# Kernel optimization log

Hardware: AMD Instinct MI355X
Metric: run time of the kernel (lower is better)

## Reference

```python
import jax, jax.numpy as jnp
import numpy as np

EPS = 1e-7
MAX_TANH = 15.0
C = 1.0  # curvature of every PoincareBall manifold in the stack

def _norm(x):
    return jnp.clip(jnp.linalg.norm(x, axis=-1, keepdims=True), EPS, None)

def _artanh(x):
    return jnp.arctanh(jnp.clip(x, -1.0 + 1e-5, 1.0 - 1e-5))

def proj(x, c=C):
    # clip points back inside the Poincare ball
    maxnorm = (1.0 - 1e-5) / jnp.sqrt(c)
    n = _norm(x)
    return jnp.where(n > maxnorm, x / n * maxnorm, x)

def expmap0(u, c=C):
    sc = jnp.sqrt(c)
    n = _norm(u)
    return jnp.tanh(jnp.clip(sc * n, -MAX_TANH, MAX_TANH)) * u / (sc * n)

def logmap0(x, c=C):
    sc = jnp.sqrt(c)
    n = _norm(x)
    return _artanh(sc * n) * x / (sc * n)

def mobius_add(x, y, c=C):
    x2 = jnp.sum(x * x, -1, keepdims=True)
    y2 = jnp.sum(y * y, -1, keepdims=True)
    xy = jnp.sum(x * y, -1, keepdims=True)
    num = (1 + 2 * c * xy + c * y2) * x + (1 - c * x2) * y
    den = 1 + 2 * c * xy + c * c * x2 * y2
    return num / jnp.clip(den, EPS, None)

def mobius_matvec(W, x, c=C):
    sc = jnp.sqrt(c)
    xn = _norm(x)
    mx = x @ W.T
    mxn = _norm(mx)
    return jnp.tanh(jnp.clip(mxn / xn * _artanh(sc * xn), -MAX_TANH, MAX_TANH)) * mx / (mxn * sc)

def hgc_layer(x, edges, node_mask, edge_mask, W, b, c_in=C, c_out=C):
    n_nodes = x.shape[0]
    # HypLinear: mobius matvec + hyperbolic bias add
    h = proj(mobius_matvec(W, x, c_in), c_in)
    hyp_bias = proj(expmap0(b[None, :], c_in), c_in)
    h = proj(mobius_add(h, hyp_bias, c_in), c_in)
    # HypAgg: masked tangent-space mean over incoming edges (gather -> segment_sum)
    row, col = edges[0], edges[1]
    ht = logmap0(h, c_in)                 # [N, d] tangent features
    msgs = ht[col] * edge_mask            # [E, d]
    agg = jax.ops.segment_sum(msgs, row, num_segments=n_nodes)
    deg = jax.ops.segment_sum(edge_mask, row, num_segments=n_nodes)
    agg = agg / jnp.clip(deg, 1.0, None)
    h = proj(expmap0(agg, c_in), c_in)
    # HypAct: nonlinearity in tangent space, re-map to output manifold
    xt = jax.nn.relu(logmap0(h, c_in))
    h = proj(expmap0(xt, c_out), c_out)
    return h * node_mask

N_NODES = 50000
N_EDGES = 1200000
DIM = 64
NUM_LAYERS = 2

def setup_inputs() -> dict:
    key = jax.random.key(0)
    ks = jax.random.split(key, 8)
    h_tan = 0.1 * jax.random.normal(ks[0], (N_NODES, DIM), dtype=jnp.float32)
    h = proj(expmap0(h_tan))  # valid Poincare-ball points
    distances = jax.random.uniform(ks[1], (N_EDGES, 1), dtype=jnp.float32)
    edges = jax.random.randint(ks[2], (2, N_EDGES), 0, N_NODES, dtype=jnp.int64)
    node_mask = jnp.ones((N_NODES, 1), dtype=jnp.float32)
    edge_mask = jnp.ones((N_EDGES, 1), dtype=jnp.float32)
    W0 = 0.1 * jax.random.normal(ks[3], (DIM, DIM), dtype=jnp.float32)
    b0 = 0.01 * jax.random.normal(ks[4], (DIM,), dtype=jnp.float32)
    W1 = 0.1 * jax.random.normal(ks[5], (DIM, DIM), dtype=jnp.float32)
    b1 = 0.01 * jax.random.normal(ks[6], (DIM,), dtype=jnp.float32)
    return {"h": h, "distances": distances, "edges": edges,
            "node_mask": node_mask, "edge_mask": edge_mask,
            "W0": W0, "b0": b0, "W1": W1, "b1": b1}

def reference(h, distances, edges, node_mask, edge_mask, W0, b0, W1, b1):
    # nn.Sequential of HyperbolicGraphConvolution layers; distances/edges/masks pass through
    out = hgc_layer(h, edges, node_mask, edge_mask, W0, b0)
    out = hgc_layer(out, edges, node_mask, edge_mask, W1, b1)
    return out
```

## Files before the change

kernel.cpp:

```cpp
#include <hip/hip_runtime.h>
#include <hip/hip_fp16.h>

#define EPS      1e-7f
#define MAX_TANH 15.0f
#define MAXNORM  0.99999f
#define ART_CLIP 0.99999f
#define HGRID    512
#define RPB      64
#define RPB_SHIFT 6
#define CAPF     2048
#define NBMAX    1024

__device__ __forceinline__ float frcp(float x) {
    return __builtin_amdgcn_rcpf(x);
}

__device__ __forceinline__ float fast_tanh_pos(float x) {
    float e = __expf(-2.0f * x);
    return (1.0f - e) * frcp(1.0f + e);
}

__device__ __forceinline__ float clamp_tanh_arg(float x) {
    return fminf(fmaxf(x, -MAX_TANH), MAX_TANH);
}

__device__ __forceinline__ float artanh_clip(float x) {
    x = fminf(fmaxf(x, -ART_CLIP), ART_CLIP);
    return 0.5f * __logf((1.0f + x) * frcp(1.0f - x));
}

__device__ __forceinline__ float gsum16(float v) {
    v += __shfl_xor(v, 1, 64);
    v += __shfl_xor(v, 2, 64);
    v += __shfl_xor(v, 4, 64);
    v += __shfl_xor(v, 8, 64);
    return v;
}

__device__ __forceinline__ void fma_h4(float4& acc, uint2 u, float m) {
    float2 f01 = __half22float2(*reinterpret_cast<__half2*>(&u.x));
    float2 f23 = __half22float2(*reinterpret_cast<__half2*>(&u.y));
    acc.x = fmaf(f01.x, m, acc.x); acc.y = fmaf(f01.y, m, acc.y);
    acc.z = fmaf(f23.x, m, acc.z); acc.w = fmaf(f23.y, m, acc.w);
}

__device__ __forceinline__ float rec_mask(unsigned v) {
    unsigned short hb = (unsigned short)(v >> 16);
    return __half2float(*reinterpret_cast<__half*>(&hb));
}

__global__ __launch_bounds__(256) void hist_kernel(
    const int* __restrict__ rows, unsigned short* __restrict__ histB,
    int n_edges, int epb, int nb)
{
    __shared__ int hh[NBMAX];
    const int b0 = blockIdx.x * epb;
    const int b1 = min(b0 + epb, n_edges);
    for (int j = threadIdx.x; j < nb; j += 256) hh[j] = 0;
    __syncthreads();
    for (int i = b0 + threadIdx.x; i < b1; i += 256)
        atomicAdd(&hh[rows[i] >> RPB_SHIFT], 1);
    __syncthreads();
    for (int j = threadIdx.x; j < nb; j += 256)
        histB[blockIdx.x * nb + j] = (unsigned short)hh[j];
}

__global__ __launch_bounds__(256, 4) void transform_kernel(
    const float* __restrict__ x, const float* __restrict__ W,
    const float* __restrict__ b, __half* __restrict__ ht, int n_nodes)
{
    __shared__ float WT[4096];
    __shared__ float xs[16 * 68];

    const int t = threadIdx.x;
    const int q = t & 15;
    const int g = t >> 4;

#pragma unroll
    for (int r = 0; r < 16; ++r) {
        int idx = r * 256 + t;
        int j = idx >> 6, k = idx & 63;
        WT[(k << 6) | (j ^ ((k & 15) << 2))] = W[idx];
    }

    float4 b4 = ((const float4*)b)[q];
    float ssb = b4.x*b4.x + b4.y*b4.y + b4.z*b4.z + b4.w*b4.w;
    float bn = fmaxf(sqrtf(gsum16(ssb)), EPS);
    float tb = fast_tanh_pos(clamp_tanh_arg(bn));
    float sb = tb * frcp(bn);
    float4 hb4 = make_float4(b4.x * sb, b4.y * sb, b4.z * sb, b4.w * sb);
    if (tb > MAXNORM) {
        float sc = MAXNORM * frcp(tb);
        hb4.x *= sc; hb4.y *= sc; hb4.z *= sc; hb4.w *= sc;
        tb = MAXNORM;
    }
    const float y2 = tb * tb;
    __syncthreads();

    const int node = blockIdx.x * 16 + g;
    const bool valid = node < n_nodes;
    const int nd = valid ? node : 0;

    float* xrow = &xs[g * 68];

    float4 x4 = ((const float4*)(x + (long long)nd * 64))[q];
    *(float4*)(xrow + (q << 2)) = x4;

    float ssx = x4.x*x4.x + x4.y*x4.y + x4.z*x4.z + x4.w*x4.w;
    float xn = fmaxf(sqrtf(gsum16(ssx)), EPS);

    float4 mxa = make_float4(0.f, 0.f, 0.f, 0.f);
    float4 mxb = make_float4(0.f, 0.f, 0.f, 0.f);
#pragma unroll
    for (int k = 0; k < 64; k += 2) {
        float xk0 = xrow[k], xk1 = xrow[k + 1];
        const float4 w0 = *(const float4*)&WT[((k    ) << 6) | ((q << 2) ^ (((k    ) & 15) << 2))];
        const float4 w1 = *(const float4*)&WT[((k + 1) << 6) | ((q << 2) ^ (((k + 1) & 15) << 2))];
        mxa.x = fmaf(w0.x, xk0, mxa.x); mxa.y = fmaf(w0.y, xk0, mxa.y);
        mxa.z = fmaf(w0.z, xk0, mxa.z); mxa.w = fmaf(w0.w, xk0, mxa.w);
        mxb.x = fmaf(w1.x, xk1, mxb.x); mxb.y = fmaf(w1.y, xk1, mxb.y);
        mxb.z = fmaf(w1.z, xk1, mxb.z); mxb.w = fmaf(w1.w, xk1, mxb.w);
    }
    float4 mx = make_float4(mxa.x + mxb.x, mxa.y + mxb.y,
                            mxa.z + mxb.z, mxa.w + mxb.w);

    float ssm = mx.x*mx.x + mx.y*mx.y + mx.z*mx.z + mx.w*mx.w;
    float mxn = fmaxf(sqrtf(gsum16(ssm)), EPS);
    float r = fast_tanh_pos(clamp_tanh_arg(mxn * frcp(xn) * artanh_clip(xn)));
    float rs = r * frcp(mxn);
    float4 hj = make_float4(mx.x * rs, mx.y * rs, mx.z * rs, mx.w * rs);
    float hn = fmaxf(r, EPS);
    if (hn > MAXNORM) {
        float sc = MAXNORM * frcp(hn);
        hj.x *= sc; hj.y *= sc; hj.z *= sc; hj.w *= sc;
        hn = MAXNORM;
    }

    float x2 = hn * hn;
    float xy = gsum16(hj.x*hb4.x + hj.y*hb4.y + hj.z*hb4.z + hj.w*hb4.w);
    float ca = 1.0f + 2.0f * xy + y2;
    float cb = 1.0f - x2;
    float iden = frcp(fmaxf(1.0f + 2.0f * xy + x2 * y2, EPS));
    hj.x = (ca * hj.x + cb * hb4.x) * iden;
    hj.y = (ca * hj.y + cb * hb4.y) * iden;
    hj.z = (ca * hj.z + cb * hb4.z) * iden;
    hj.w = (ca * hj.w + cb * hb4.w) * iden;

    float ssh = hj.x*hj.x + hj.y*hj.y + hj.z*hj.z + hj.w*hj.w;
    float hn2 = fmaxf(sqrtf(gsum16(ssh)), EPS);
    float sc2 = (hn2 > MAXNORM) ? (MAXNORM * frcp(hn2)) : 1.0f;
    float hnc = fminf(hn2, MAXNORM);
    float lr = artanh_clip(hnc) * frcp(hnc) * sc2;
    hj.x *= lr; hj.y *= lr; hj.z *= lr; hj.w *= lr;

    if (valid) {
        __half2 p01 = __float22half2_rn(make_float2(hj.x, hj.y));
        __half2 p23 = __float22half2_rn(make_float2(hj.z, hj.w));
        uint2 o;
        o.x = *reinterpret_cast<unsigned*>(&p01);
        o.y = *reinterpret_cast<unsigned*>(&p23);
        *((uint2*)(ht + (long long)node * 64) + q) = o;
    }
}

__global__ __launch_bounds__(HGRID) void scan_bucket_kernel(
    unsigned short* __restrict__ histB, int* __restrict__ tot, int nb)
{
    __shared__ int wsum[8];
    const int b = blockIdx.x;
    const int t = threadIdx.x;
    const int lane = t & 63, wid = t >> 6;
    int v = histB[t * nb + b];
    int incl = v;
#pragma unroll
    for (int o = 1; o < 64; o <<= 1) {
        int tt = __shfl_up(incl, o, 64);
        if (lane >= o) incl += tt;
    }
    if (lane == 63) wsum[wid] = incl;
    __syncthreads();
    if (wid == 0 && lane < 8) {
        int ws = wsum[lane];
#pragma unroll
        for (int o = 1; o < 8; o <<= 1) {
            int tt = __shfl_up(ws, o, 64);
            if (lane >= o) ws += tt;
        }
        wsum[lane] = ws;
    }
    __syncthreads();
    int base = (wid > 0) ? wsum[wid - 1] : 0;
    histB[t * nb + b] = (unsigned short)(base + incl - v);
    if (t == HGRID - 1) tot[b] = base + incl;
}

__global__ __launch_bounds__(NBMAX) void scan_base_kernel(
    const int* __restrict__ tot, int* __restrict__ bucket_base, int nb)
{
    __shared__ int s[NBMAX];
    const int t = threadIdx.x;
    int v = (t < nb) ? tot[t] : 0;
    s[t] = v;
    __syncthreads();
    for (int off = 1; off < NBMAX; off <<= 1) {
        int u = (t >= off) ? s[t - off] : 0;
        __syncthreads();
        s[t] += u;
        __syncthreads();
    }
    if (t < nb) bucket_base[t] = s[t] - v;
    if (t == nb - 1) bucket_base[nb] = s[t];
}

__global__ __launch_bounds__(256) void coarse_scatter_kernel(
    const int* __restrict__ rows, const int* __restrict__ cols,
    const float* __restrict__ edge_mask, const unsigned short* __restrict__ off,
    const int* __restrict__ bucket_base,
    int2* __restrict__ coarse, int n_edges, int epb, int nb)
{
    __shared__ int cur[NBMAX];
    const int b0 = blockIdx.x * epb;
    const int b1 = min(b0 + epb, n_edges);
    for (int j = threadIdx.x; j < nb; j += 256)
        cur[j] = bucket_base[j] + (int)off[blockIdx.x * nb + j];
    __syncthreads();
    for (int i = b0 + threadIdx.x; i < b1; i += 256) {
        int r = rows[i], c = cols[i];
        float m = edge_mask[i];
        int pos = atomicAdd(&cur[r >> RPB_SHIFT], 1);
        coarse[pos] = make_int2((r << 16) | c, __float_as_int(m));
    }
}

__global__ __launch_bounds__(512) void fine_gather_kernel(
    const int2* __restrict__ coarse, const int* __restrict__ bucket_base,
    const __half* __restrict__ ht1, const float* __restrict__ node_mask,
    const float* __restrict__ W, const float* __restrict__ bvec,
    unsigned* __restrict__ csr4, int* __restrict__ row_start,
    __half* __restrict__ ht2, int n_nodes, int n_edges)
{
    __shared__ int hh[RPB], incl[RPB], curs[RPB];
    __shared__ unsigned outE[CAPF];
    __shared__ float WT[4096];
    __shared__ float xs[32 * 68];

    const int t = threadIdx.x;
    const int b = blockIdx.x;
    const int q = t & 15;
    const int g = t >> 4;
    const int bbase = bucket_base[b];
    const int n_e = bucket_base[b + 1] - bbase;

#pragma unroll
    for (int r = 0; r < 8; ++r) {
        int idx = r * 512 + t;
        int j = idx >> 6, k = idx & 63;
        WT[(k << 6) | (j ^ ((k & 15) << 2))] = W[idx];
    }
    float4 b4 = ((const float4*)bvec)[q];
    float ssb = b4.x*b4.x + b4.y*b4.y + b4.z*b4.z + b4.w*b4.w;
    float bn = fmaxf(sqrtf(gsum16(ssb)), EPS);
    float tb = fast_tanh_pos(clamp_tanh_arg(bn));
    float sb = tb * frcp(bn);
    float4 hb4 = make_float4(b4.x * sb, b4.y * sb, b4.z * sb, b4.w * sb);
    if (tb > MAXNORM) {
        float sc = MAXNORM * frcp(tb);
        hb4.x *= sc; hb4.y *= sc; hb4.z *= sc; hb4.w *= sc;
        tb = MAXNORM;
    }
    const float y2 = tb * tb;

    if (t < RPB) hh[t] = 0;
    __syncthreads();
    int2 regs[4];
#pragma unroll
    for (int k = 0; k < 4; ++k) {
        int i = t + k * 512;
        if (i < n_e) {
            regs[k] = coarse[bbase + i];
            atomicAdd(&hh[(regs[k].x >> 16) & (RPB - 1)], 1);
        }
    }
    __syncthreads();
    if (t < 64) {
        int v = hh[t];
        int inc = v;
#pragma unroll
        for (int o = 1; o < 64; o <<= 1) {
            int tt = __shfl_up(inc, o, 64);
            if (t >= o) inc += tt;
        }
        incl[t] = inc;
        curs[t] = inc - v;
        int grow = (b << RPB_SHIFT) + t;
        if (grow < n_nodes) row_start[grow] = bbase + inc - v;
    }
    if (b == gridDim.x - 1 && t == 0) row_start[n_nodes] = n_edges;
    __syncthreads();
#pragma unroll
    for (int k = 0; k < 4; ++k) {
        int i = t + k * 512;
        if (i < n_e) {
            int slot = atomicAdd(&curs[(regs[k].x >> 16) & (RPB - 1)], 1);
            if (slot < CAPF) {
                __half hm = __float2half(__int_as_float(regs[k].y));
                outE[slot] = (unsigned)(regs[k].x & 0xffff) |
                             ((unsigned)*reinterpret_cast<unsigned short*>(&hm) << 16);
            }
        }
    }
    __syncthreads();

    const int lim = min(n_e, CAPF);
    for (int i = t; i < lim; i += 512)
        csr4[bbase + i] = outE[i];

    const uint2* __restrict__ htq = (const uint2*)ht1 + q;

#pragma unroll
    for (int batch = 0; batch < 2; ++batch) {
        const int ln = batch * 32 + g;
        const int node = (b << RPB_SHIFT) + ln;
        const bool valid = node < n_nodes;
        const int nd = valid ? node : (n_nodes - 1);
        const int s0 = incl[ln] - hh[ln];
        const int e0 = incl[ln];

        float4 acc = make_float4(0.f, 0.f, 0.f, 0.f);
        float msum = 0.f;
        int j = s0;
        for (; j + 8 <= e0; j += 8) {
            unsigned v0 = outE[j    ], v1 = outE[j + 1], v2 = outE[j + 2], v3 = outE[j + 3];
            unsigned v4 = outE[j + 4], v5 = outE[j + 5], v6 = outE[j + 6], v7 = outE[j + 7];
            uint2 u0 = htq[(v0 & 0xffffu) * 16u];
            uint2 u1 = htq[(v1 & 0xffffu) * 16u];
            uint2 u2 = htq[(v2 & 0xffffu) * 16u];
            uint2 u3 = htq[(v3 & 0xffffu) * 16u];
            uint2 u4 = htq[(v4 & 0xffffu) * 16u];
            uint2 u5 = htq[(v5 & 0xffffu) * 16u];
            uint2 u6 = htq[(v6 & 0xffffu) * 16u];
            uint2 u7 = htq[(v7 & 0xffffu) * 16u];
            float m0 = rec_mask(v0), m1 = rec_mask(v1);
            float m2 = rec_mask(v2), m3 = rec_mask(v3);
            float m4 = rec_mask(v4), m5 = rec_mask(v5);
            float m6 = rec_mask(v6), m7 = rec_mask(v7);
            fma_h4(acc, u0, m0); fma_h4(acc, u1, m1);
            fma_h4(acc, u2, m2); fma_h4(acc, u3, m3);
            fma_h4(acc, u4, m4); fma_h4(acc, u5, m5);
            fma_h4(acc, u6, m6); fma_h4(acc, u7, m7);
            msum += (m0 + m1 + m2 + m3) + (m4 + m5 + m6 + m7);
        }
        for (; j + 4 <= e0; j += 4) {
            unsigned v0 = outE[j], v1 = outE[j + 1], v2 = outE[j + 2], v3 = outE[j + 3];
            uint2 u0 = htq[(v0 & 0xffffu) * 16u];
            uint2 u1 = htq[(v1 & 0xffffu) * 16u];
            uint2 u2 = htq[(v2 & 0xffffu) * 16u];
            uint2 u3 = htq[(v3 & 0xffffu) * 16u];
            float m0 = rec_mask(v0), m1 = rec_mask(v1);
            float m2 = rec_mask(v2), m3 = rec_mask(v3);
            fma_h4(acc, u0, m0); fma_h4(acc, u1, m1);
            fma_h4(acc, u2, m2); fma_h4(acc, u3, m3);
            msum += m0 + m1 + m2 + m3;
        }
        for (; j < e0; ++j) {
            unsigned v = outE[j];
            uint2 u = htq[(v & 0xffffu) * 16u];
            float m = rec_mask(v);
            fma_h4(acc, u, m);
            msum += m;
        }

        const float inv = frcp(fmaxf(msum, 1.0f));
        acc.x *= inv; acc.y *= inv; acc.z *= inv; acc.w *= inv;

        float ss = acc.x*acc.x + acc.y*acc.y + acc.z*acc.z + acc.w*acc.w;
        float n1 = fmaxf(sqrtf(gsum16(ss)), EPS);
        float t1 = fast_tanh_pos(clamp_tanh_arg(n1));
        float r1 = t1 * frcp(n1);
        acc.x *= r1; acc.y *= r1; acc.z *= r1; acc.w *= r1;
        if (t1 > MAXNORM) {
            float sc = MAXNORM * frcp(t1);
            acc.x *= sc; acc.y *= sc; acc.z *= sc; acc.w *= sc;
            t1 = MAXNORM;
        }
        float n2 = fmaxf(t1, EPS);
        float r2s = artanh_clip(n2) * frcp(n2);
        acc.x = fmaxf(acc.x * r2s, 0.f); acc.y = fmaxf(acc.y * r2s, 0.f);
        acc.z = fmaxf(acc.z * r2s, 0.f); acc.w = fmaxf(acc.w * r2s, 0.f);

        ss = acc.x*acc.x + acc.y*acc.y + acc.z*acc.z + acc.w*acc.w;
        float n3 = fmaxf(sqrtf(gsum16(ss)), EPS);
        float t3 = fast_tanh_pos(clamp_tanh_arg(n3));
        float r3 = t3 * frcp(n3);
        acc.x *= r3; acc.y *= r3; acc.z *= r3; acc.w *= r3;
        if (t3 > MAXNORM) {
            float sc = MAXNORM * frcp(t3);
            acc.x *= sc; acc.y *= sc; acc.z *= sc; acc.w *= sc;
            t3 = MAXNORM;
        }

        const float nm = node_mask[nd];
        acc.x *= nm; acc.y *= nm; acc.z *= nm; acc.w *= nm;

        float* xrow = &xs[g * 68];
        *(float4*)(xrow + (q << 2)) = acc;

        float4 mxa = make_float4(0.f, 0.f, 0.f, 0.f);
        float4 mxb = make_float4(0.f, 0.f, 0.f, 0.f);
#pragma unroll
        for (int k = 0; k < 64; k += 2) {
            float xk0 = xrow[k], xk1 = xrow[k + 1];
            const float4 w0 = *(const float4*)&WT[((k    ) << 6) | ((q << 2) ^ (((k    ) & 15) << 2))];
            const float4 w1 = *(const float4*)&WT[((k + 1) << 6) | ((q << 2) ^ (((k + 1) & 15) << 2))];
            mxa.x = fmaf(w0.x, xk0, mxa.x); mxa.y = fmaf(w0.y, xk0, mxa.y);
            mxa.z = fmaf(w0.z, xk0, mxa.z); mxa.w = fmaf(w0.w, xk0, mxa.w);
            mxb.x = fmaf(w1.x, xk1, mxb.x); mxb.y = fmaf(w1.y, xk1, mxb.y);
            mxb.z = fmaf(w1.z, xk1, mxb.z); mxb.w = fmaf(w1.w, xk1, mxb.w);
        }
        float4 mx = make_float4(mxa.x + mxb.x, mxa.y + mxb.y,
                                mxa.z + mxb.z, mxa.w + mxb.w);

        float xn  = fmaxf(t3 * fabsf(nm), EPS);
        float ssm = mx.x*mx.x + mx.y*mx.y + mx.z*mx.z + mx.w*mx.w;
        float mxn = fmaxf(sqrtf(gsum16(ssm)), EPS);
        float r = fast_tanh_pos(clamp_tanh_arg(mxn * frcp(xn) * artanh_clip(xn)));
        float rs = r * frcp(mxn);
        float4 hj = make_float4(mx.x * rs, mx.y * rs, mx.z * rs, mx.w * rs);
        float hn = fmaxf(r, EPS);
        if (hn > MAXNORM) {
            float sc = MAXNORM * frcp(hn);
            hj.x *= sc; hj.y *= sc; hj.z *= sc; hj.w *= sc;
            hn = MAXNORM;
        }

        float x2 = hn * hn;
        float xy = gsum16(hj.x*hb4.x + hj.y*hb4.y + hj.z*hb4.z + hj.w*hb4.w);
        float ca = 1.0f + 2.0f * xy + y2;
        float cb = 1.0f - x2;
        float iden = frcp(fmaxf(1.0f + 2.0f * xy + x2 * y2, EPS));
        hj.x = (ca * hj.x + cb * hb4.x) * iden;
        hj.y = (ca * hj.y + cb * hb4.y) * iden;
        hj.z = (ca * hj.z + cb * hb4.z) * iden;
        hj.w = (ca * hj.w + cb * hb4.w) * iden;

        float ssh = hj.x*hj.x + hj.y*hj.y + hj.z*hj.z + hj.w*hj.w;
        float hn2 = fmaxf(sqrtf(gsum16(ssh)), EPS);
        float sc2 = (hn2 > MAXNORM) ? (MAXNORM * frcp(hn2)) : 1.0f;
        float hnc = fminf(hn2, MAXNORM);
        float lr = artanh_clip(hnc) * frcp(hnc) * sc2;
        hj.x *= lr; hj.y *= lr; hj.z *= lr; hj.w *= lr;

        if (valid) {
            __half2 p01 = __float22half2_rn(make_float2(hj.x, hj.y));
            __half2 p23 = __float22half2_rn(make_float2(hj.z, hj.w));
            uint2 o;
            o.x = *reinterpret_cast<unsigned*>(&p01);
            o.y = *reinterpret_cast<unsigned*>(&p23);
            *((uint2*)(ht2 + (long long)node * 64) + q) = o;
        }
    }
}

__global__ __launch_bounds__(256) void gather2_kernel(
    const __half* __restrict__ ht, const unsigned* __restrict__ csr4,
    const int* __restrict__ row_start, const float* __restrict__ node_mask,
    float* __restrict__ outp, int n_nodes)
{
    const int t = threadIdx.x;
    const int lane = t & 63;
    const int wv = t >> 6;
    const int ns = lane >> 4;
    const int q  = lane & 15;

    const int node = blockIdx.x * 16 + (wv << 2) + ns;
    const bool valid = node < n_nodes;
    const int nd = valid ? node : (n_nodes - 1);
    const int s = row_start[nd];
    const int e = row_start[nd + 1];

    const uint2* __restrict__ htq = (const uint2*)ht + q;

    float4 acc = make_float4(0.f, 0.f, 0.f, 0.f);
    float msum = 0.f;
    int j = s;
    for (; j + 8 <= e; j += 8) {
        unsigned v0 = csr4[j    ], v1 = csr4[j + 1], v2 = csr4[j + 2], v3 = csr4[j + 3];
        unsigned v4 = csr4[j + 4], v5 = csr4[j + 5], v6 = csr4[j + 6], v7 = csr4[j + 7];
        uint2 u0 = htq[(v0 & 0xffffu) * 16u];
        uint2 u1 = htq[(v1 & 0xffffu) * 16u];
        uint2 u2 = htq[(v2 & 0xffffu) * 16u];
        uint2 u3 = htq[(v3 & 0xffffu) * 16u];
        uint2 u4 = htq[(v4 & 0xffffu) * 16u];
        uint2 u5 = htq[(v5 & 0xffffu) * 16u];
        uint2 u6 = htq[(v6 & 0xffffu) * 16u];
        uint2 u7 = htq[(v7 & 0xffffu) * 16u];
        float m0 = rec_mask(v0), m1 = rec_mask(v1);
        float m2 = rec_mask(v2), m3 = rec_mask(v3);
        float m4 = rec_mask(v4), m5 = rec_mask(v5);
        float m6 = rec_mask(v6), m7 = rec_mask(v7);
        fma_h4(acc, u0, m0); fma_h4(acc, u1, m1);
        fma_h4(acc, u2, m2); fma_h4(acc, u3, m3);
        fma_h4(acc, u4, m4); fma_h4(acc, u5, m5);
        fma_h4(acc, u6, m6); fma_h4(acc, u7, m7);
        msum += (m0 + m1 + m2 + m3) + (m4 + m5 + m6 + m7);
    }
    for (; j + 4 <= e; j += 4) {
        unsigned v0 = csr4[j], v1 = csr4[j + 1], v2 = csr4[j + 2], v3 = csr4[j + 3];
        uint2 u0 = htq[(v0 & 0xffffu) * 16u];
        uint2 u1 = htq[(v1 & 0xffffu) * 16u];
        uint2 u2 = htq[(v2 & 0xffffu) * 16u];
        uint2 u3 = htq[(v3 & 0xffffu) * 16u];
        float m0 = rec_mask(v0), m1 = rec_mask(v1);
        float m2 = rec_mask(v2), m3 = rec_mask(v3);
        fma_h4(acc, u0, m0); fma_h4(acc, u1, m1);
        fma_h4(acc, u2, m2); fma_h4(acc, u3, m3);
        msum += m0 + m1 + m2 + m3;
    }
    for (; j < e; ++j) {
        unsigned v = csr4[j];
        uint2 u = htq[(v & 0xffffu) * 16u];
        float m = rec_mask(v);
        fma_h4(acc, u, m);
        msum += m;
    }

    const float inv = frcp(fmaxf(msum, 1.0f));
    acc.x *= inv; acc.y *= inv; acc.z *= inv; acc.w *= inv;

    float ss = acc.x*acc.x + acc.y*acc.y + acc.z*acc.z + acc.w*acc.w;
    float n1 = fmaxf(sqrtf(gsum16(ss)), EPS);
    float t1 = fast_tanh_pos(clamp_tanh_arg(n1));
    float r1 = t1 * frcp(n1);
    acc.x *= r1; acc.y *= r1; acc.z *= r1; acc.w *= r1;
    if (t1 > MAXNORM) {
        float sc = MAXNORM * frcp(t1);
        acc.x *= sc; acc.y *= sc; acc.z *= sc; acc.w *= sc;
        t1 = MAXNORM;
    }
    float n2 = fmaxf(t1, EPS);
    float r2 = artanh_clip(n2) * frcp(n2);
    acc.x = fmaxf(acc.x * r2, 0.f); acc.y = fmaxf(acc.y * r2, 0.f);
    acc.z = fmaxf(acc.z * r2, 0.f); acc.w = fmaxf(acc.w * r2, 0.f);

    ss = acc.x*acc.x + acc.y*acc.y + acc.z*acc.z + acc.w*acc.w;
    float n3 = fmaxf(sqrtf(gsum16(ss)), EPS);
    float t3 = fast_tanh_pos(clamp_tanh_arg(n3));
    float r3 = t3 * frcp(n3);
    acc.x *= r3; acc.y *= r3; acc.z *= r3; acc.w *= r3;
    if (t3 > MAXNORM) {
        float sc = MAXNORM * frcp(t3);
        acc.x *= sc; acc.y *= sc; acc.z *= sc; acc.w *= sc;
        t3 = MAXNORM;
    }

    const float nm = node_mask[nd];
    acc.x *= nm; acc.y *= nm; acc.z *= nm; acc.w *= nm;

    if (valid) ((float4*)(outp + (long long)node * 64))[q] = acc;
}

extern "C" void kernel_launch(void* const* d_in, const int* in_sizes, int n_in,
                              void* d_out, int out_size, void* d_ws, size_t ws_size,
                              hipStream_t stream) {
    const float* h         = (const float*)d_in[0];
    const int*   edges     = (const int*)d_in[2];
    const float* node_mask = (const float*)d_in[3];
    const float* edge_mask = (const float*)d_in[4];
    const float* W0        = (const float*)d_in[5];
    const float* b0        = (const float*)d_in[6];
    const float* W1        = (const float*)d_in[7];
    const float* b1        = (const float*)d_in[8];
    float* out = (float*)d_out;

    const int N = in_sizes[0] / 64;
    const int E = in_sizes[4];
    const int* rows = edges;
    const int* cols = edges + E;

    const int NB  = (N + RPB - 1) / RPB;
    const int EPB = (E + HGRID - 1) / HGRID;

    size_t nd = (size_t)N * 64;
    char* ws = (char*)d_ws;
    __half*   B1          = (__half*)ws;   ws += nd * sizeof(__half);
    __half*   B2          = (__half*)ws;   ws += nd * sizeof(__half);
    int2*     coarse      = (int2*)ws;     ws += (size_t)E * sizeof(int2);
    unsigned* csr4        = (unsigned*)ws; ws += (size_t)E * sizeof(unsigned);
    unsigned short* histB = (unsigned short*)ws;
    ws += (size_t)HGRID * NB * sizeof(unsigned short);
    int*      tot         = (int*)ws;      ws += (size_t)NB * sizeof(int);
    int*      bucket_base = (int*)ws;      ws += (size_t)(NB + 1) * sizeof(int);
    int*      row_start   = (int*)ws;      ws += (size_t)(N + 1) * sizeof(int);

    const int TB = (N + 15) / 16;
    const int NGRID = (N + 15) / 16;

    hist_kernel<<<HGRID, 256, 0, stream>>>(rows, histB, E, EPB, NB);

    transform_kernel<<<TB, 256, 0, stream>>>(h, W0, b0, B1, N);

    scan_bucket_kernel<<<NB, HGRID, 0, stream>>>(histB, tot, NB);
    scan_base_kernel<<<1, NBMAX, 0, stream>>>(tot, bucket_base, NB);

    coarse_scatter_kernel<<<HGRID, 256, 0, stream>>>(
        rows, cols, edge_mask, histB, bucket_base, coarse, E, EPB, NB);

    fine_gather_kernel<<<NB, 512, 0, stream>>>(
        coarse, bucket_base, B1, node_mask, W1, b1, csr4, row_start, B2, N, E);

    gather2_kernel<<<NGRID, 256, 0, stream>>>(
        B2, csr4, row_start, node_mask, out, N);
}
```

Measured before the change: 195.9 us.

## Replace bucketed two-pass CSR build with global atomic count/scan/scatter

Replaces the hierarchical bucket histogram plus coarse scatter plus in-LDS fine sort with a direct per-node count using global atomics, a three-kernel prefix scan, and a global-atomic scatter into CSR. The first-layer gather, previously fused with the fine sort, becomes a standalone gather1 kernel that reads the CSR, mirroring gather2. This removes the intermediate coarse buffer and shared-memory bucketing. In exchange it adds heavy global atomic contention on per-node counters and cursors, scatters edges in nondeterministic order, and adds more kernel launches.

```diff
diff --git a/kernel.cpp b/kernel.cpp
--- a/kernel.cpp
+++ b/kernel.cpp
@@ -5,11 +5,6 @@
 #define MAX_TANH 15.0f
 #define MAXNORM  0.99999f
 #define ART_CLIP 0.99999f
-#define HGRID    512
-#define RPB      64
-#define RPB_SHIFT 6
-#define CAPF     2048
-#define NBMAX    1024
 
 __device__ __forceinline__ float frcp(float x) {
     return __builtin_amdgcn_rcpf(x);
@@ -49,20 +44,80 @@
     return __half2float(*reinterpret_cast<__half*>(&hb));
 }
 
-__global__ __launch_bounds__(256) void hist_kernel(
-    const int* __restrict__ rows, unsigned short* __restrict__ histB,
-    int n_edges, int epb, int nb)
-{
-    __shared__ int hh[NBMAX];
-    const int b0 = blockIdx.x * epb;
-    const int b1 = min(b0 + epb, n_edges);
-    for (int j = threadIdx.x; j < nb; j += 256) hh[j] = 0;
+__global__ __launch_bounds__(256) void zero_kernel(int* __restrict__ p, int n)
+{
+    int i = blockIdx.x * 256 + threadIdx.x;
+    if (i < n) p[i] = 0;
+}
+
+__global__ __launch_bounds__(256) void count_kernel(
+    const int* __restrict__ rows, int* __restrict__ cnt, int n_edges)
+{
+    const int stride = gridDim.x * 256;
+    for (int i = blockIdx.x * 256 + threadIdx.x; i < n_edges; i += stride)
+        atomicAdd(&cnt[rows[i]], 1);
+}
+
+__global__ __launch_bounds__(1024) void scanA_kernel(
+    const int* __restrict__ cnt, int* __restrict__ rs,
+    int* __restrict__ partial, int n)
+{
+    __shared__ int s[1024];
+    const int t = threadIdx.x;
+    const int i = blockIdx.x * 1024 + t;
+    int v = (i < n) ? cnt[i] : 0;
+    s[t] = v;
     __syncthreads();
-    for (int i = b0 + threadIdx.x; i < b1; i += 256)
-        atomicAdd(&hh[rows[i] >> RPB_SHIFT], 1);
-    __syncthreads();
-    for (int j = threadIdx.x; j < nb; j += 256)
-        histB[blockIdx.x * nb + j] = (unsigned short)hh[j];
+    for (int off = 1; off < 1024; off <<= 1) {
+        int u = (t >= off) ? s[t - off] : 0;
+        __syncthreads();
+        s[t] += u;
+        __syncthreads();
+    }
+    if (i < n) rs[i] = s[t] - v;
+    if (t == 1023) partial[blockIdx.x] = s[1023];
+}
+
+__global__ __launch_bounds__(64) void scanB_kernel(
+    int* __restrict__ partial, int nch)
+{
+    const int t = threadIdx.x;
+    int v = (t < nch) ? partial[t] : 0;
+    int inc = v;
+#pragma unroll
+    for (int o = 1; o < 64; o <<= 1) {
+        int u = __shfl_up(inc, o, 64);
+        if (t >= o) inc += u;
+    }
+    if (t < nch) partial[t] = inc - v;
+}
+
+__global__ __launch_bounds__(256) void scanC_kernel(
+    int* __restrict__ rs, int* __restrict__ cursor,
+    const int* __restrict__ partial, int n, int e)
+{
+    int i = blockIdx.x * 256 + threadIdx.x;
+    if (i < n) {
+        int r = rs[i] + partial[i >> 10];
+        rs[i] = r;
+        cursor[i] = r;
+    }
+    if (i == 0) rs[n] = e;
+}
+
+__global__ __launch_bounds__(256) void scatter_kernel(
+    const int* __restrict__ rows, const int* __restrict__ cols,
+    const float* __restrict__ edge_mask, int* __restrict__ cursor,
+    unsigned* __restrict__ csr4, int n_edges)
+{
+    const int stride = gridDim.x * 256;
+    for (int i = blockIdx.x * 256 + threadIdx.x; i < n_edges; i += stride) {
+        int r = rows[i], c = cols[i];
+        __half hm = __float2half(edge_mask[i]);
+        int pos = atomicAdd(&cursor[r], 1);
+        csr4[pos] = (unsigned)c |
+                    ((unsigned)*reinterpret_cast<unsigned short*>(&hm) << 16);
+    }
 }
 
 __global__ __launch_bounds__(256, 4) void transform_kernel(
@@ -163,97 +218,22 @@
     }
 }
 
-__global__ __launch_bounds__(HGRID) void scan_bucket_kernel(
-    unsigned short* __restrict__ histB, int* __restrict__ tot, int nb)
-{
-    __shared__ int wsum[8];
-    const int b = blockIdx.x;
+__global__ __launch_bounds__(256) void gather1_kernel(
+    const __half* __restrict__ ht1, const unsigned* __restrict__ csr4,
+    const int* __restrict__ row_start, const float* __restrict__ node_mask,
+    const float* __restrict__ W, const float* __restrict__ bvec,
+    __half* __restrict__ ht2, int n_nodes)
+{
+    __shared__ float WT[4096];
+    __shared__ float xs[16 * 68];
+
     const int t = threadIdx.x;
-    const int lane = t & 63, wid = t >> 6;
-    int v = histB[t * nb + b];
-    int incl = v;
-#pragma unroll
-    for (int o = 1; o < 64; o <<= 1) {
-        int tt = __shfl_up(incl, o, 64);
-        if (lane >= o) incl += tt;
-    }
-    if (lane == 63) wsum[wid] = incl;
-    __syncthreads();
-    if (wid == 0 && lane < 8) {
-        int ws = wsum[lane];
-#pragma unroll
-        for (int o = 1; o < 8; o <<= 1) {
-            int tt = __shfl_up(ws, o, 64);
-            if (lane >= o) ws += tt;
-        }
-        wsum[lane] = ws;
-    }
-    __syncthreads();
-    int base = (wid > 0) ? wsum[wid - 1] : 0;
-    histB[t * nb + b] = (unsigned short)(base + incl - v);
-    if (t == HGRID - 1) tot[b] = base + incl;
-}
-
-__global__ __launch_bounds__(NBMAX) void scan_base_kernel(
-    const int* __restrict__ tot, int* __restrict__ bucket_base, int nb)
-{
-    __shared__ int s[NBMAX];
-    const int t = threadIdx.x;
-    int v = (t < nb) ? tot[t] : 0;
-    s[t] = v;
-    __syncthreads();
-    for (int off = 1; off < NBMAX; off <<= 1) {
-        int u = (t >= off) ? s[t - off] : 0;
-        __syncthreads();
-        s[t] += u;
-        __syncthreads();
-    }
-    if (t < nb) bucket_base[t] = s[t] - v;
-    if (t == nb - 1) bucket_base[nb] = s[t];
-}
-
-__global__ __launch_bounds__(256) void coarse_scatter_kernel(
-    const int* __restrict__ rows, const int* __restrict__ cols,
-    const float* __restrict__ edge_mask, const unsigned short* __restrict__ off,
-    const int* __restrict__ bucket_base,
-    int2* __restrict__ coarse, int n_edges, int epb, int nb)
-{
-    __shared__ int cur[NBMAX];
-    const int b0 = blockIdx.x * epb;
-    const int b1 = min(b0 + epb, n_edges);
-    for (int j = threadIdx.x; j < nb; j += 256)
-        cur[j] = bucket_base[j] + (int)off[blockIdx.x * nb + j];
-    __syncthreads();
-    for (int i = b0 + threadIdx.x; i < b1; i += 256) {
-        int r = rows[i], c = cols[i];
-        float m = edge_mask[i];
-        int pos = atomicAdd(&cur[r >> RPB_SHIFT], 1);
-        coarse[pos] = make_int2((r << 16) | c, __float_as_int(m));
-    }
-}
-
-__global__ __launch_bounds__(512) void fine_gather_kernel(
-    const int2* __restrict__ coarse, const int* __restrict__ bucket_base,
-    const __half* __restrict__ ht1, const float* __restrict__ node_mask,
-    const float* __restrict__ W, const float* __restrict__ bvec,
-    unsigned* __restrict__ csr4, int* __restrict__ row_start,
-    __half* __restrict__ ht2, int n_nodes, int n_edges)
-{
-    __shared__ int hh[RPB], incl[RPB], curs[RPB];
-    __shared__ unsigned outE[CAPF];
-    __shared__ float WT[4096];
-    __shared__ float xs[32 * 68];
-
-    const int t = threadIdx.x;
-    const int b = blockIdx.x;
     const int q = t & 15;
     const int g = t >> 4;
-    const int bbase = bucket_base[b];
-    const int n_e = bucket_base[b + 1] - bbase;
 
 #pragma unroll
-    for (int r = 0; r < 8; ++r) {
-        int idx = r * 512 + t;
+    for (int r = 0; r < 16; ++r) {
+        int idx = r * 256 + t;
         int j = idx >> 6, k = idx & 63;
         WT[(k << 6) | (j ^ ((k & 15) << 2))] = W[idx];
     }
@@ -269,216 +249,15 @@
         tb = MAXNORM;
     }
     const float y2 = tb * tb;
-
-    if (t < RPB) hh[t] = 0;
     __syncthreads();
-    int2 regs[4];
-#pragma unroll
-    for (int k = 0; k < 4; ++k) {
-        int i = t + k * 512;
-        if (i < n_e) {
-            regs[k] = coarse[bbase + i];
-            atomicAdd(&hh[(regs[k].x >> 16) & (RPB - 1)], 1);
-        }
-    }
-    __syncthreads();
-    if (t < 64) {
-        int v = hh[t];
-        int inc = v;
-#pragma unroll
-        for (int o = 1; o < 64; o <<= 1) {
-            int tt = __shfl_up(inc, o, 64);
-            if (t >= o) inc += tt;
-        }
-        incl[t] = inc;
-        curs[t] = inc - v;
-        int grow = (b << RPB_SHIFT) + t;
-        if (grow < n_nodes) row_start[grow] = bbase + inc - v;
-    }
-    if (b == gridDim.x - 1 && t == 0) row_start[n_nodes] = n_edges;
-    __syncthreads();
-#pragma unroll
-    for (int k = 0; k < 4; ++k) {
-        int i = t + k * 512;
-        if (i < n_e) {
-            int slot = atomicAdd(&curs[(regs[k].x >> 16) & (RPB - 1)], 1);
-            if (slot < CAPF) {
-                __half hm = __float2half(__int_as_float(regs[k].y));
-                outE[slot] = (unsigned)(regs[k].x & 0xffff) |
-                             ((unsigned)*reinterpret_cast<unsigned short*>(&hm) << 16);
-            }
-        }
-    }
-    __syncthreads();
-
-    const int lim = min(n_e, CAPF);
-    for (int i = t; i < lim; i += 512)
-        csr4[bbase + i] = outE[i];
-
-    const uint2* __restrict__ htq = (const uint2*)ht1 + q;
-
-#pragma unroll
-    for (int batch = 0; batch < 2; ++batch) {
-        const int ln = batch * 32 + g;
-        const int node = (b << RPB_SHIFT) + ln;
-        const bool valid = node < n_nodes;
-        const int nd = valid ? node : (n_nodes - 1);
-        const int s0 = incl[ln] - hh[ln];
-        const int e0 = incl[ln];
-
-        float4 acc = make_float4(0.f, 0.f, 0.f, 0.f);
-        float msum = 0.f;
-        int j = s0;
-        for (; j + 8 <= e0; j += 8) {
-            unsigned v0 = outE[j    ], v1 = outE[j + 1], v2 = outE[j + 2], v3 = outE[j + 3];
-            unsigned v4 = outE[j + 4], v5 = outE[j + 5], v6 = outE[j + 6], v7 = outE[j + 7];
-            uint2 u0 = htq[(v0 & 0xffffu) * 16u];
-            uint2 u1 = htq[(v1 & 0xffffu) * 16u];
-            uint2 u2 = htq[(v2 & 0xffffu) * 16u];
-            uint2 u3 = htq[(v3 & 0xffffu) * 16u];
-            uint2 u4 = htq[(v4 & 0xffffu) * 16u];
-            uint2 u5 = htq[(v5 & 0xffffu) * 16u];
-            uint2 u6 = htq[(v6 & 0xffffu) * 16u];
-            uint2 u7 = htq[(v7 & 0xffffu) * 16u];
-            float m0 = rec_mask(v0), m1 = rec_mask(v1);
-            float m2 = rec_mask(v2), m3 = rec_mask(v3);
-            float m4 = rec_mask(v4), m5 = rec_mask(v5);
-            float m6 = rec_mask(v6), m7 = rec_mask(v7);
-            fma_h4(acc, u0, m0); fma_h4(acc, u1, m1);
-            fma_h4(acc, u2, m2); fma_h4(acc, u3, m3);
-            fma_h4(acc, u4, m4); fma_h4(acc, u5, m5);
-            fma_h4(acc, u6, m6); fma_h4(acc, u7, m7);
-            msum += (m0 + m1 + m2 + m3) + (m4 + m5 + m6 + m7);
-        }
-        for (; j + 4 <= e0; j += 4) {
-            unsigned v0 = outE[j], v1 = outE[j + 1], v2 = outE[j + 2], v3 = outE[j + 3];
-            uint2 u0 = htq[(v0 & 0xffffu) * 16u];
-            uint2 u1 = htq[(v1 & 0xffffu) * 16u];
-            uint2 u2 = htq[(v2 & 0xffffu) * 16u];
-            uint2 u3 = htq[(v3 & 0xffffu) * 16u];
-            float m0 = rec_mask(v0), m1 = rec_mask(v1);
-            float m2 = rec_mask(v2), m3 = rec_mask(v3);
-            fma_h4(acc, u0, m0); fma_h4(acc, u1, m1);
-            fma_h4(acc, u2, m2); fma_h4(acc, u3, m3);
-            msum += m0 + m1 + m2 + m3;
-        }
-        for (; j < e0; ++j) {
-            unsigned v = outE[j];
-            uint2 u = htq[(v & 0xffffu) * 16u];
-            float m = rec_mask(v);
-            fma_h4(acc, u, m);
-            msum += m;
-        }
-
-        const float inv = frcp(fmaxf(msum, 1.0f));
-        acc.x *= inv; acc.y *= inv; acc.z *= inv; acc.w *= inv;
-
-        float ss = acc.x*acc.x + acc.y*acc.y + acc.z*acc.z + acc.w*acc.w;
-        float n1 = fmaxf(sqrtf(gsum16(ss)), EPS);
-        float t1 = fast_tanh_pos(clamp_tanh_arg(n1));
-        float r1 = t1 * frcp(n1);
-        acc.x *= r1; acc.y *= r1; acc.z *= r1; acc.w *= r1;
-        if (t1 > MAXNORM) {
-            float sc = MAXNORM * frcp(t1);
-            acc.x *= sc; acc.y *= sc; acc.z *= sc; acc.w *= sc;
-            t1 = MAXNORM;
-        }
-        float n2 = fmaxf(t1, EPS);
-        float r2s = artanh_clip(n2) * frcp(n2);
-        acc.x = fmaxf(acc.x * r2s, 0.f); acc.y = fmaxf(acc.y * r2s, 0.f);
-        acc.z = fmaxf(acc.z * r2s, 0.f); acc.w = fmaxf(acc.w * r2s, 0.f);
-
-        ss = acc.x*acc.x + acc.y*acc.y + acc.z*acc.z + acc.w*acc.w;
-        float n3 = fmaxf(sqrtf(gsum16(ss)), EPS);
-        float t3 = fast_tanh_pos(clamp_tanh_arg(n3));
-        float r3 = t3 * frcp(n3);
-        acc.x *= r3; acc.y *= r3; acc.z *= r3; acc.w *= r3;
-        if (t3 > MAXNORM) {
-            float sc = MAXNORM * frcp(t3);
-            acc.x *= sc; acc.y *= sc; acc.z *= sc; acc.w *= sc;
-            t3 = MAXNORM;
-        }
-
-        const float nm = node_mask[nd];
-        acc.x *= nm; acc.y *= nm; acc.z *= nm; acc.w *= nm;
-
-        float* xrow = &xs[g * 68];
-        *(float4*)(xrow + (q << 2)) = acc;
-
-        float4 mxa = make_float4(0.f, 0.f, 0.f, 0.f);
-        float4 mxb = make_float4(0.f, 0.f, 0.f, 0.f);
-#pragma unroll
-        for (int k = 0; k < 64; k += 2) {
-            float xk0 = xrow[k], xk1 = xrow[k + 1];
-            const float4 w0 = *(const float4*)&WT[((k    ) << 6) | ((q << 2) ^ (((k    ) & 15) << 2))];
-            const float4 w1 = *(const float4*)&WT[((k + 1) << 6) | ((q << 2) ^ (((k + 1) & 15) << 2))];
-            mxa.x = fmaf(w0.x, xk0, mxa.x); mxa.y = fmaf(w0.y, xk0, mxa.y);
-            mxa.z = fmaf(w0.z, xk0, mxa.z); mxa.w = fmaf(w0.w, xk0, mxa.w);
-            mxb.x = fmaf(w1.x, xk1, mxb.x); mxb.y = fmaf(w1.y, xk1, mxb.y);
-            mxb.z = fmaf(w1.z, xk1, mxb.z); mxb.w = fmaf(w1.w, xk1, mxb.w);
-        }
-        float4 mx = make_float4(mxa.x + mxb.x, mxa.y + mxb.y,
-                                mxa.z + mxb.z, mxa.w + mxb.w);
-
-        float xn  = fmaxf(t3 * fabsf(nm), EPS);
-        float ssm = mx.x*mx.x + mx.y*mx.y + mx.z*mx.z + mx.w*mx.w;
-        float mxn = fmaxf(sqrtf(gsum16(ssm)), EPS);
-        float r = fast_tanh_pos(clamp_tanh_arg(mxn * frcp(xn) * artanh_clip(xn)));
-        float rs = r * frcp(mxn);
-        float4 hj = make_float4(mx.x * rs, mx.y * rs, mx.z * rs, mx.w * rs);
-        float hn = fmaxf(r, EPS);
-        if (hn > MAXNORM) {
-            float sc = MAXNORM * frcp(hn);
-            hj.x *= sc; hj.y *= sc; hj.z *= sc; hj.w *= sc;
-            hn = MAXNORM;
-        }
-
-        float x2 = hn * hn;
-        float xy = gsum16(hj.x*hb4.x + hj.y*hb4.y + hj.z*hb4.z + hj.w*hb4.w);
-        float ca = 1.0f + 2.0f * xy + y2;
-        float cb = 1.0f - x2;
-        float iden = frcp(fmaxf(1.0f + 2.0f * xy + x2 * y2, EPS));
-        hj.x = (ca * hj.x + cb * hb4.x) * iden;
-        hj.y = (ca * hj.y + cb * hb4.y) * iden;
-        hj.z = (ca * hj.z + cb * hb4.z) * iden;
-        hj.w = (ca * hj.w + cb * hb4.w) * iden;
-
-        float ssh = hj.x*hj.x + hj.y*hj.y + hj.z*hj.z + hj.w*hj.w;
-        float hn2 = fmaxf(sqrtf(gsum16(ssh)), EPS);
-        float sc2 = (hn2 > MAXNORM) ? (MAXNORM * frcp(hn2)) : 1.0f;
-        float hnc = fminf(hn2, MAXNORM);
-        float lr = artanh_clip(hnc) * frcp(hnc) * sc2;
-        hj.x *= lr; hj.y *= lr; hj.z *= lr; hj.w *= lr;
-
-        if (valid) {
-            __half2 p01 = __float22half2_rn(make_float2(hj.x, hj.y));
-            __half2 p23 = __float22half2_rn(make_float2(hj.z, hj.w));
-            uint2 o;
-            o.x = *reinterpret_cast<unsigned*>(&p01);
-            o.y = *reinterpret_cast<unsigned*>(&p23);
-            *((uint2*)(ht2 + (long long)node * 64) + q) = o;
-        }
-    }
-}
-
-__global__ __launch_bounds__(256) void gather2_kernel(
-    const __half* __restrict__ ht, const unsigned* __restrict__ csr4,
-    const int* __restrict__ row_start, const float* __restrict__ node_mask,
-    float* __restrict__ outp, int n_nodes)
-{
-    const int t = threadIdx.x;
-    const int lane = t & 63;
-    const int wv = t >> 6;
-    const int ns = lane >> 4;
-    const int q  = lane & 15;
-
-    const int node = blockIdx.x * 16 + (wv << 2) + ns;
+
+    const int node = blockIdx.x * 16 + g;
     const bool valid = node < n_nodes;
     const int nd = valid ? node : (n_nodes - 1);
     const int s = row_start[nd];
     const int e = row_start[nd + 1];
 
-    const uint2* __restrict__ htq = (const uint2*)ht + q;
+    const uint2* __restrict__ htq = (const uint2*)ht1 + q;
 
     float4 acc = make_float4(0.f, 0.f, 0.f, 0.f);
     float msum = 0.f;
@@ -538,6 +317,159 @@
         t1 = MAXNORM;
     }
     float n2 = fmaxf(t1, EPS);
+    float r2s = artanh_clip(n2) * frcp(n2);
+    acc.x = fmaxf(acc.x * r2s, 0.f); acc.y = fmaxf(acc.y * r2s, 0.f);
+    acc.z = fmaxf(acc.z * r2s, 0.f); acc.w = fmaxf(acc.w * r2s, 0.f);
+
+    ss = acc.x*acc.x + acc.y*acc.y + acc.z*acc.z + acc.w*acc.w;
+    float n3 = fmaxf(sqrtf(gsum16(ss)), EPS);
+    float t3 = fast_tanh_pos(clamp_tanh_arg(n3));
+    float r3 = t3 * frcp(n3);
+    acc.x *= r3; acc.y *= r3; acc.z *= r3; acc.w *= r3;
+    if (t3 > MAXNORM) {
+        float sc = MAXNORM * frcp(t3);
+        acc.x *= sc; acc.y *= sc; acc.z *= sc; acc.w *= sc;
+        t3 = MAXNORM;
+    }
+
+    const float nm = node_mask[nd];
+    acc.x *= nm; acc.y *= nm; acc.z *= nm; acc.w *= nm;
+
+    float* xrow = &xs[g * 68];
+    *(float4*)(xrow + (q << 2)) = acc;
+
+    float4 mxa = make_float4(0.f, 0.f, 0.f, 0.f);
+    float4 mxb = make_float4(0.f, 0.f, 0.f, 0.f);
+#pragma unroll
+    for (int k = 0; k < 64; k += 2) {
+        float xk0 = xrow[k], xk1 = xrow[k + 1];
+        const float4 w0 = *(const float4*)&WT[((k    ) << 6) | ((q << 2) ^ (((k    ) & 15) << 2))];
+        const float4 w1 = *(const float4*)&WT[((k + 1) << 6) | ((q << 2) ^ (((k + 1) & 15) << 2))];
+        mxa.x = fmaf(w0.x, xk0, mxa.x); mxa.y = fmaf(w0.y, xk0, mxa.y);
+        mxa.z = fmaf(w0.z, xk0, mxa.z); mxa.w = fmaf(w0.w, xk0, mxa.w);
+        mxb.x = fmaf(w1.x, xk1, mxb.x); mxb.y = fmaf(w1.y, xk1, mxb.y);
+        mxb.z = fmaf(w1.z, xk1, mxb.z); mxb.w = fmaf(w1.w, xk1, mxb.w);
+    }
+    float4 mx = make_float4(mxa.x + mxb.x, mxa.y + mxb.y,
+                            mxa.z + mxb.z, mxa.w + mxb.w);
+
+    float xn  = fmaxf(t3 * fabsf(nm), EPS);
+    float ssm = mx.x*mx.x + mx.y*mx.y + mx.z*mx.z + mx.w*mx.w;
+    float mxn = fmaxf(sqrtf(gsum16(ssm)), EPS);
+    float r = fast_tanh_pos(clamp_tanh_arg(mxn * frcp(xn) * artanh_clip(xn)));
+    float rs = r * frcp(mxn);
+    float4 hj = make_float4(mx.x * rs, mx.y * rs, mx.z * rs, mx.w * rs);
+    float hn = fmaxf(r, EPS);
+    if (hn > MAXNORM) {
+        float sc = MAXNORM * frcp(hn);
+        hj.x *= sc; hj.y *= sc; hj.z *= sc; hj.w *= sc;
+        hn = MAXNORM;
+    }
+
+    float x2 = hn * hn;
+    float xy = gsum16(hj.x*hb4.x + hj.y*hb4.y + hj.z*hb4.z + hj.w*hb4.w);
+    float ca = 1.0f + 2.0f * xy + y2;
+    float cb = 1.0f - x2;
+    float iden = frcp(fmaxf(1.0f + 2.0f * xy + x2 * y2, EPS));
+    hj.x = (ca * hj.x + cb * hb4.x) * iden;
+    hj.y = (ca * hj.y + cb * hb4.y) * iden;
+    hj.z = (ca * hj.z + cb * hb4.z) * iden;
+    hj.w = (ca * hj.w + cb * hb4.w) * iden;
+
+    float ssh = hj.x*hj.x + hj.y*hj.y + hj.z*hj.z + hj.w*hj.w;
+    float hn2 = fmaxf(sqrtf(gsum16(ssh)), EPS);
+    float sc2 = (hn2 > MAXNORM) ? (MAXNORM * frcp(hn2)) : 1.0f;
+    float hnc = fminf(hn2, MAXNORM);
+    float lr = artanh_clip(hnc) * frcp(hnc) * sc2;
+    hj.x *= lr; hj.y *= lr; hj.z *= lr; hj.w *= lr;
+
+    if (valid) {
+        __half2 p01 = __float22half2_rn(make_float2(hj.x, hj.y));
+        __half2 p23 = __float22half2_rn(make_float2(hj.z, hj.w));
+        uint2 o;
+        o.x = *reinterpret_cast<unsigned*>(&p01);
+        o.y = *reinterpret_cast<unsigned*>(&p23);
+        *((uint2*)(ht2 + (long long)node * 64) + q) = o;
+    }
+}
+
+__global__ __launch_bounds__(256) void gather2_kernel(
+    const __half* __restrict__ ht, const unsigned* __restrict__ csr4,
+    const int* __restrict__ row_start, const float* __restrict__ node_mask,
+    float* __restrict__ outp, int n_nodes)
+{
+    const int t = threadIdx.x;
+    const int lane = t & 63;
+    const int wv = t >> 6;
+    const int ns = lane >> 4;
+    const int q  = lane & 15;
+
+    const int node = blockIdx.x * 16 + (wv << 2) + ns;
+    const bool valid = node < n_nodes;
+    const int nd = valid ? node : (n_nodes - 1);
+    const int s = row_start[nd];
+    const int e = row_start[nd + 1];
+
+    const uint2* __restrict__ htq = (const uint2*)ht + q;
+
+    float4 acc = make_float4(0.f, 0.f, 0.f, 0.f);
+    float msum = 0.f;
+    int j = s;
+    for (; j + 8 <= e; j += 8) {
+        unsigned v0 = csr4[j    ], v1 = csr4[j + 1], v2 = csr4[j + 2], v3 = csr4[j + 3];
+        unsigned v4 = csr4[j + 4], v5 = csr4[j + 5], v6 = csr4[j + 6], v7 = csr4[j + 7];
+        uint2 u0 = htq[(v0 & 0xffffu) * 16u];
+        uint2 u1 = htq[(v1 & 0xffffu) * 16u];
+        uint2 u2 = htq[(v2 & 0xffffu) * 16u];
+        uint2 u3 = htq[(v3 & 0xffffu) * 16u];
+        uint2 u4 = htq[(v4 & 0xffffu) * 16u];
+        uint2 u5 = htq[(v5 & 0xffffu) * 16u];
+        uint2 u6 = htq[(v6 & 0xffffu) * 16u];
+        uint2 u7 = htq[(v7 & 0xffffu) * 16u];
+        float m0 = rec_mask(v0), m1 = rec_mask(v1);
+        float m2 = rec_mask(v2), m3 = rec_mask(v3);
+        float m4 = rec_mask(v4), m5 = rec_mask(v5);
+        float m6 = rec_mask(v6), m7 = rec_mask(v7);
+        fma_h4(acc, u0, m0); fma_h4(acc, u1, m1);
+        fma_h4(acc, u2, m2); fma_h4(acc, u3, m3);
+        fma_h4(acc, u4, m4); fma_h4(acc, u5, m5);
+        fma_h4(acc, u6, m6); fma_h4(acc, u7, m7);
+        msum += (m0 + m1 + m2 + m3) + (m4 + m5 + m6 + m7);
+    }
+    for (; j + 4 <= e; j += 4) {
+        unsigned v0 = csr4[j], v1 = csr4[j + 1], v2 = csr4[j + 2], v3 = csr4[j + 3];
+        uint2 u0 = htq[(v0 & 0xffffu) * 16u];
+        uint2 u1 = htq[(v1 & 0xffffu) * 16u];
+        uint2 u2 = htq[(v2 & 0xffffu) * 16u];
+        uint2 u3 = htq[(v3 & 0xffffu) * 16u];
+        float m0 = rec_mask(v0), m1 = rec_mask(v1);
+        float m2 = rec_mask(v2), m3 = rec_mask(v3);
+        fma_h4(acc, u0, m0); fma_h4(acc, u1, m1);
+        fma_h4(acc, u2, m2); fma_h4(acc, u3, m3);
+        msum += m0 + m1 + m2 + m3;
+    }
+    for (; j < e; ++j) {
+        unsigned v = csr4[j];
+        uint2 u = htq[(v & 0xffffu) * 16u];
+        float m = rec_mask(v);
+        fma_h4(acc, u, m);
+        msum += m;
+    }
+
+    const float inv = frcp(fmaxf(msum, 1.0f));
+    acc.x *= inv; acc.y *= inv; acc.z *= inv; acc.w *= inv;
+
+    float ss = acc.x*acc.x + acc.y*acc.y + acc.z*acc.z + acc.w*acc.w;
+    float n1 = fmaxf(sqrtf(gsum16(ss)), EPS);
+    float t1 = fast_tanh_pos(clamp_tanh_arg(n1));
+    float r1 = t1 * frcp(n1);
+    acc.x *= r1; acc.y *= r1; acc.z *= r1; acc.w *= r1;
+    if (t1 > MAXNORM) {
+        float sc = MAXNORM * frcp(t1);
+        acc.x *= sc; acc.y *= sc; acc.z *= sc; acc.w *= sc;
+        t1 = MAXNORM;
+    }
+    float n2 = fmaxf(t1, EPS);
     float r2 = artanh_clip(n2) * frcp(n2);
     acc.x = fmaxf(acc.x * r2, 0.f); acc.y = fmaxf(acc.y * r2, 0.f);
     acc.z = fmaxf(acc.z * r2, 0.f); acc.w = fmaxf(acc.w * r2, 0.f);
@@ -577,36 +509,34 @@
     const int* rows = edges;
     const int* cols = edges + E;
 
-    const int NB  = (N + RPB - 1) / RPB;
-    const int EPB = (E + HGRID - 1) / HGRID;
-
     size_t nd = (size_t)N * 64;
     char* ws = (char*)d_ws;
-    __half*   B1          = (__half*)ws;   ws += nd * sizeof(__half);
-    __half*   B2          = (__half*)ws;   ws += nd * sizeof(__half);
-    int2*     coarse      = (int2*)ws;     ws += (size_t)E * sizeof(int2);
-    unsigned* csr4        = (unsigned*)ws; ws += (size_t)E * sizeof(unsigned);
-    unsigned short* histB = (unsigned short*)ws;
-    ws += (size_t)HGRID * NB * sizeof(unsigned short);
-    int*      tot         = (int*)ws;      ws += (size_t)NB * sizeof(int);
-    int*      bucket_base = (int*)ws;      ws += (size_t)(NB + 1) * sizeof(int);
-    int*      row_start   = (int*)ws;      ws += (size_t)(N + 1) * sizeof(int);
-
-    const int TB = (N + 15) / 16;
+    __half*   B1        = (__half*)ws;   ws += nd * sizeof(__half);
+    __half*   B2        = (__half*)ws;   ws += nd * sizeof(__half);
+    unsigned* csr4      = (unsigned*)ws; ws += (size_t)E * sizeof(unsigned);
+    int*      cnt       = (int*)ws;      ws += (size_t)N * sizeof(int);
+    int*      cursor    = (int*)ws;      ws += (size_t)N * sizeof(int);
+    int*      row_start = (int*)ws;      ws += (size_t)(N + 1) * sizeof(int);
+    int*      partial   = (int*)ws;      ws += 64 * sizeof(int);
+
+    const int NCH   = (N + 1023) / 1024;
     const int NGRID = (N + 15) / 16;
 
-    hist_kernel<<<HGRID, 256, 0, stream>>>(rows, histB, E, EPB, NB);
-
-    transform_kernel<<<TB, 256, 0, stream>>>(h, W0, b0, B1, N);
-
-    scan_bucket_kernel<<<NB, HGRID, 0, stream>>>(histB, tot, NB);
-    scan_base_kernel<<<1, NBMAX, 0, stream>>>(tot, bucket_base, NB);
-
-    coarse_scatter_kernel<<<HGRID, 256, 0, stream>>>(
-        rows, cols, edge_mask, histB, bucket_base, coarse, E, EPB, NB);
-
-    fine_gather_kernel<<<NB, 512, 0, stream>>>(
-        coarse, bucket_base, B1, node_mask, W1, b1, csr4, row_start, B2, N, E);
+    zero_kernel<<<(N + 255) / 256, 256, 0, stream>>>(cnt, N);
+    count_kernel<<<1024, 256, 0, stream>>>(rows, cnt, E);
+
+    transform_kernel<<<NGRID, 256, 0, stream>>>(h, W0, b0, B1, N);
+
+    scanA_kernel<<<NCH, 1024, 0, stream>>>(cnt, row_start, partial, N);
+    scanB_kernel<<<1, 64, 0, stream>>>(partial, NCH);
+    scanC_kernel<<<(N + 255) / 256, 256, 0, stream>>>(
+        row_start, cursor, partial, N, E);
+
+    scatter_kernel<<<1024, 256, 0, stream>>>(
+        rows, cols, edge_mask, cursor, csr4, E);
+
+    gather1_kernel<<<NGRID, 256, 0, stream>>>(
+        B1, csr4, row_start, node_mask, W1, b1, B2, N);
 
     gather2_kernel<<<NGRID, 256, 0, stream>>>(
         B2, csr4, row_start, node_mask, out, N);
```

New measurement: 317.6 us. 62.1% more time.
